# Kernel optimization log

Measured on AMD Instinct MI355X. Metric: run time of the kernel, lower is better.

## Reference

```python
import jax, jax.numpy as jnp
import numpy as np

RES = 14
KEY_DIM = 32
NUM_HEADS = 12
ATTN_RATIO = 4
DIM = 384
VAL_ATTN_DIM = ATTN_RATIO * KEY_DIM * NUM_HEADS  # 1536
QKV_DIM = VAL_ATTN_DIM + 2 * KEY_DIM * NUM_HEADS  # 2304
BN_EPS = 1e-5


def _bias_idxs():
    # torch.meshgrid default is 'ij'
    gy, gx = jnp.meshgrid(jnp.arange(RES), jnp.arange(RES), indexing='ij')
    pos = jnp.stack([gy.reshape(-1), gx.reshape(-1)])           # [2, N]
    rel = jnp.abs(pos[:, :, None] - pos[:, None, :])            # [2, N, N]
    return rel[0] * RES + rel[1]                                # [N, N] int


def _linear_bn(x, w, gamma, beta, mean, var):
    # bias-free Linear (torch weight layout [out,in]) + BatchNorm1d (eval)
    y = x @ w.T
    inv = gamma / jnp.sqrt(var + BN_EPS)
    return y * inv + (beta - mean * inv)


def setup_inputs() -> dict:
    key = jax.random.key(0)
    ks = jax.random.split(key, 12)
    B, N = 128, RES * RES
    f = jax.random.normal
    return {
        'x': f(ks[0], (B, N, DIM), jnp.float32),
        'qkv_w': f(ks[1], (QKV_DIM, DIM), jnp.float32) * 0.02,
        'qkv_gamma': f(ks[2], (QKV_DIM,), jnp.float32) * 0.1 + 1.0,
        'qkv_beta': f(ks[3], (QKV_DIM,), jnp.float32) * 0.1,
        'qkv_mean': f(ks[4], (QKV_DIM,), jnp.float32) * 0.1,
        'qkv_var': jax.random.uniform(ks[5], (QKV_DIM,), jnp.float32, 0.5, 1.5),
        'attn_biases': f(ks[6], (NUM_HEADS, RES * RES), jnp.float32) * 0.1,
        'proj_w': f(ks[7], (DIM, VAL_ATTN_DIM), jnp.float32) * 0.02,
        'proj_gamma': f(ks[8], (DIM,), jnp.float32) * 0.1 + 1.0,
        'proj_beta': f(ks[9], (DIM,), jnp.float32) * 0.1,
        'proj_mean': f(ks[10], (DIM,), jnp.float32) * 0.1,
        'proj_var': jax.random.uniform(ks[11], (DIM,), jnp.float32, 0.5, 1.5),
    }


def reference(x, qkv_w, qkv_gamma, qkv_beta, qkv_mean, qkv_var,
              attn_biases, proj_w, proj_gamma, proj_beta, proj_mean, proj_var):
    B, N, _ = x.shape
    scale = KEY_DIM ** -0.5
    qkv = _linear_bn(x, qkv_w, qkv_gamma, qkv_beta, qkv_mean, qkv_var)
    qkv = qkv.reshape(B, N, NUM_HEADS, -1)
    q = qkv[..., :KEY_DIM]                       # [B,N,H,dk]
    k = qkv[..., KEY_DIM:2 * KEY_DIM]            # [B,N,H,dk]
    v = qkv[..., 2 * KEY_DIM:]                   # [B,N,H,dv]
    bias = attn_biases[:, _bias_idxs()]          # [H,N,N]
    attn = jnp.einsum('bnhd,bmhd->bhnm', q, k) * scale + bias[None]
    attn = jax.nn.softmax(attn, axis=-1)
    out = jnp.einsum('bhnm,bmhd->bnhd', attn, v).reshape(B, N, VAL_ATTN_DIM)
    out = jax.nn.silu(out)
    return _linear_bn(out, proj_w, proj_gamma, proj_beta, proj_mean, proj_var)
```

## Files before the change

kernel.cpp:

```cpp
#include <hip/hip_runtime.h>
#include <cstdint>

#define NQ 196
#define DIMX 384
#define QKVD 2304
#define VAD 1536
#define NHD 12
#define MTOT 25088

#define KSTR 40
#define VSTR 232

typedef unsigned int u32;
typedef unsigned short u16;
typedef __bf16 bf16_t;
typedef bf16_t bf16x8 __attribute__((ext_vector_type(8)));
typedef float f32x4 __attribute__((ext_vector_type(4)));

__device__ inline u16 f2b(float f) {
  u32 u = __float_as_uint(f);
  u32 r = (u + 0x7fffu + ((u >> 16) & 1u)) >> 16;
  return (u16)r;
}
__device__ inline float b2f(u16 u) { return __uint_as_float(((u32)u) << 16); }
__device__ inline int iabs(int v) { return v < 0 ? -v : v; }

__device__ inline void gld_lds16(const void* g, void* l) {
  __builtin_amdgcn_global_load_lds((__attribute__((address_space(1))) void*)g,
                                   (__attribute__((address_space(3))) void*)l,
                                   16, 0, 0);
}


__global__ void cvt_kernel(const float* __restrict__ in, u16* __restrict__ out, int n4) {
  int i = blockIdx.x * 256 + threadIdx.x;
  if (i >= n4) return;
  float4 v = ((const float4*)in)[i];
  ushort4 o;
  o.x = f2b(v.x); o.y = f2b(v.y); o.z = f2b(v.z); o.w = f2b(v.w);
  ((ushort4*)out)[i] = o;
}

__global__ void bn_tab(const float* __restrict__ g, const float* __restrict__ be,
                       const float* __restrict__ mn, const float* __restrict__ vr,
                       float* __restrict__ inv, float* __restrict__ off, int n) {
  int i = blockIdx.x * 256 + threadIdx.x;
  if (i >= n) return;
  float iv = g[i] * rsqrtf(vr[i] + 1e-5f);
  inv[i] = iv;
  off[i] = be[i] - mn[i] * iv;
}


template <int MODE>
__global__ __launch_bounds__(256) void gemm_bt(
    const u16* __restrict__ A, const u16* __restrict__ B, int K,
    const float* __restrict__ inv, const float* __restrict__ off,
    u16* __restrict__ Qb, u16* __restrict__ Kb, u16* __restrict__ Vt,
    float* __restrict__ out) {
  __shared__ __align__(16) u16 As[128 * 32];
  __shared__ __align__(16) u16 Bs[128 * 32];
  const int tid = threadIdx.x;
  const int wid = tid >> 6, lane = tid & 63;
  const int wm = wid & 1, wn = wid >> 1;
  const int fr = lane & 15, fk = (lane >> 4) << 3;
  const u16* Ab = A + (size_t)(blockIdx.y * 128) * K;
  const u16* Bb = B + (size_t)(blockIdx.x * 128) * K;
  const int c0 = (wid << 6) | lane;
  const int r0 = c0 >> 2, kc0 = (c0 & 3) << 3;
  const int c1 = c0 + 256;
  const int r1 = c1 >> 2, kc1 = (c1 & 3) << 3;

  f32x4 acc[4][4] = {};

  for (int k0 = 0; k0 < K; k0 += 32) {
    gld_lds16(Ab + (size_t)r0 * K + (k0 + kc0), &As[wid << 9]);
    gld_lds16(Ab + (size_t)r1 * K + (k0 + kc1), &As[2048 + (wid << 9)]);
    gld_lds16(Bb + (size_t)r0 * K + (k0 + kc0), &Bs[wid << 9]);
    gld_lds16(Bb + (size_t)r1 * K + (k0 + kc1), &Bs[2048 + (wid << 9)]);
    __syncthreads();
    bf16x8 av[4], bv[4];
#pragma unroll
    for (int t = 0; t < 4; t++)
      av[t] = *(const bf16x8*)&As[(wm * 64 + t * 16 + fr) * 32 + fk];
#pragma unroll
    for (int t = 0; t < 4; t++)
      bv[t] = *(const bf16x8*)&Bs[(wn * 64 + t * 16 + fr) * 32 + fk];
#pragma unroll
    for (int mt = 0; mt < 4; mt++)
#pragma unroll
      for (int nt = 0; nt < 4; nt++)
        acc[mt][nt] = __builtin_amdgcn_mfma_f32_16x16x32_bf16(av[mt], bv[nt], acc[mt][nt], 0, 0, 0);
    __syncthreads();
  }

  const int colb = blockIdx.x * 128 + wn * 64 + fr;
  const int rowb = blockIdx.y * 128 + wm * 64 + ((lane >> 4) << 2);
#pragma unroll
  for (int nt = 0; nt < 4; nt++) {
    const int col = colb + nt * 16;
    const float iv = inv[col], of = off[col];
    if (MODE == 0) {
      const int h = col / 192, r = col - h * 192;
#pragma unroll
      for (int mt = 0; mt < 4; mt++)
#pragma unroll
        for (int rg = 0; rg < 4; rg++) {
          const int row = rowb + mt * 16 + rg;
          const float v = acc[mt][nt][rg] * iv + of;
          const int b = row / 196, n = row - b * 196;
          const size_t bh = (size_t)(b * NHD + h);
          const u16 us = f2b(v);
          if (r < 32) Qb[(bh * NQ + n) * 32 + r] = us;
          else if (r < 64) Kb[(bh * NQ + n) * 32 + (r - 32)] = us;
          else Vt[(bh * 128 + (r - 64)) * NQ + n] = us;
        }
    } else {
#pragma unroll
      for (int mt = 0; mt < 4; mt++)
#pragma unroll
        for (int rg = 0; rg < 4; rg++) {
          const int row = rowb + mt * 16 + rg;
          out[(size_t)row * DIMX + col] = acc[mt][nt][rg] * iv + of;
        }
    }
  }
}


__global__ __launch_bounds__(512) void attn_kernel(
    const u16* __restrict__ Qg, const u16* __restrict__ Kg,
    const u16* __restrict__ Vtg, const float* __restrict__ biases,
    u16* __restrict__ AO) {
  __shared__ __align__(16) u16 Ks[208 * KSTR];
  __shared__ __align__(16) u16 Vs[128 * VSTR];
  __shared__ __align__(16) u16 Ps[8][16 * VSTR];
  __shared__ __align__(16) float biasS[NQ];

  const int tid = threadIdx.x, wid = tid >> 6, lane = tid & 63;
  const int fr = lane & 15, fj = lane >> 4, fk = fj << 3;
  const int bh = blockIdx.x, b = bh / NHD, h = bh - b * NHD;
  const float scale = 0.17677669529663687f;

  for (int i = tid; i < NQ * 4; i += 512) {
    const int m = i >> 2, kc = (i & 3) << 3;
    uint4 v = *(const uint4*)(Kg + ((size_t)bh * NQ + m) * 32 + kc);
    *(uint4*)&Ks[m * KSTR + kc] = v;
  }
  {
    const u32* src = (const u32*)(Vtg + (size_t)bh * 128 * NQ);
    u32* dst = (u32*)Vs;
    for (int i = tid; i < 128 * 98; i += 512) {
      const int d = i / 98, nc = i - d * 98;
      dst[d * (VSTR / 2) + nc] = src[i];
    }
    for (int i = tid; i < 128 * 18; i += 512) {
      const int d = i / 18, nc = 98 + (i - d * 18);
      dst[d * (VSTR / 2) + nc] = 0u;
    }
  }
  if (tid < NQ) biasS[tid] = biases[h * NQ + tid];
  {
    const int row = lane >> 2, c = 208 + (lane & 3) * 4;
    *(uint2*)&Ps[wid][row * VSTR + c] = make_uint2(0u, 0u);
  }
  __syncthreads();

  for (int rt = wid; rt < 13; rt += 8) {
    int qrow = rt * 16 + fr; qrow = qrow > 195 ? 195 : qrow;
    const bf16x8 qf = *(const bf16x8*)(Qg + ((size_t)bh * NQ + qrow) * 32 + fk);

    f32x4 s[13];
#pragma unroll
    for (int t = 0; t < 13; t++) {
      const bf16x8 kf = *(const bf16x8*)&Ks[(t * 16 + fr) * KSTR + fk];
      f32x4 z = {0.f, 0.f, 0.f, 0.f};
      s[t] = __builtin_amdgcn_mfma_f32_16x16x32_bf16(qf, kf, z, 0, 0, 0);
    }

    int yn[4], xn[4];
#pragma unroll
    for (int rg = 0; rg < 4; rg++) {
      int n = rt * 16 + fj * 4 + rg;
      int y = (n * 586) >> 13; y = y > 13 ? 13 : y;
      yn[rg] = y; xn[rg] = n - y * 14;
    }
#pragma unroll
    for (int t = 0; t < 13; t++) {
      const int m = t * 16 + fr;
      const bool valid = m < NQ;
      int ym = (m * 586) >> 13; ym = ym > 13 ? 13 : ym;
      const int xm = m - ym * 14;
#pragma unroll
      for (int rg = 0; rg < 4; rg++) {
        int idx = iabs(yn[rg] - ym) * 14 + iabs(xn[rg] - xm);
        idx = idx > 195 ? 195 : idx;
        const float bv = biasS[idx];
        s[t][rg] = valid ? (s[t][rg] * scale + bv) : -1e30f;
      }
    }
    float rinv[4];
#pragma unroll
    for (int rg = 0; rg < 4; rg++) {
      float mx = s[0][rg];
#pragma unroll
      for (int t = 1; t < 13; t++) mx = fmaxf(mx, s[t][rg]);
      mx = fmaxf(mx, __shfl_xor(mx, 1));
      mx = fmaxf(mx, __shfl_xor(mx, 2));
      mx = fmaxf(mx, __shfl_xor(mx, 4));
      mx = fmaxf(mx, __shfl_xor(mx, 8));
      float ls = 0.f;
#pragma unroll
      for (int t = 0; t < 13; t++) {
        const float e = __expf(s[t][rg] - mx);
        s[t][rg] = e;
        ls += e;
      }
      ls += __shfl_xor(ls, 1);
      ls += __shfl_xor(ls, 2);
      ls += __shfl_xor(ls, 4);
      ls += __shfl_xor(ls, 8);
      rinv[rg] = 1.f / ls;
    }
#pragma unroll
    for (int t = 0; t < 13; t++)
#pragma unroll
      for (int rg = 0; rg < 4; rg++)
        Ps[wid][(fj * 4 + rg) * VSTR + t * 16 + fr] = f2b(s[t][rg]);
    __threadfence_block();

    f32x4 o[8] = {};
#pragma unroll
    for (int kc = 0; kc < 7; kc++) {
      const bf16x8 pf = *(const bf16x8*)&Ps[wid][fr * VSTR + kc * 32 + fk];
#pragma unroll
      for (int dt = 0; dt < 8; dt++) {
        const bf16x8 vf = *(const bf16x8*)&Vs[(dt * 16 + fr) * VSTR + kc * 32 + fk];
        o[dt] = __builtin_amdgcn_mfma_f32_16x16x32_bf16(pf, vf, o[dt], 0, 0, 0);
      }
    }
#pragma unroll
    for (int rg = 0; rg < 4; rg++) {
      const int n = rt * 16 + fj * 4 + rg;
      if (n < NQ) {
        const float rv = rinv[rg];
#pragma unroll
        for (int dt = 0; dt < 8; dt++) {
          float x = o[dt][rg] * rv;
          x = x / (1.f + __expf(-x));
          AO[((size_t)(b * NQ + n)) * VAD + h * 128 + dt * 16 + fr] = f2b(x);
        }
      }
    }
    __threadfence_block();
  }
}


extern "C" void kernel_launch(void* const* d_in, const int* in_sizes, int n_in,
                              void* d_out, int out_size, void* d_ws, size_t ws_size,
                              hipStream_t stream) {
  const float* x          = (const float*)d_in[0];
  const float* qkv_w      = (const float*)d_in[1];
  const float* qkv_gamma  = (const float*)d_in[2];
  const float* qkv_beta   = (const float*)d_in[3];
  const float* qkv_mean   = (const float*)d_in[4];
  const float* qkv_var    = (const float*)d_in[5];
  const float* attn_bias  = (const float*)d_in[6];
  const float* proj_w     = (const float*)d_in[7];
  const float* proj_gamma = (const float*)d_in[8];
  const float* proj_beta  = (const float*)d_in[9];
  const float* proj_mean  = (const float*)d_in[10];
  const float* proj_var   = (const float*)d_in[11];

  const size_t szXB    = (size_t)MTOT * DIMX * 2;
  const size_t szQKVW  = (size_t)QKVD * DIMX * 2;
  const size_t szPROJW = (size_t)DIMX * VAD * 2;
  const size_t szQK    = (size_t)128 * NHD * NQ * 32 * 2;
  const size_t szV     = (size_t)128 * NHD * 128 * NQ * 2;
  const size_t szAO    = (size_t)MTOT * VAD * 2;
  const size_t szX     = (szXB + szQKVW > szAO) ? (szXB + szQKVW) : szAO;

  char* w = (char*)d_ws;
  u16* projwb = (u16*)w; w += szPROJW;
  float* inv1 = (float*)w; w += QKVD * 4;
  float* off1 = (float*)w; w += QKVD * 4;
  float* inv2 = (float*)w; w += DIMX * 4;
  float* off2 = (float*)w; w += DIMX * 4;
  u16* Qb = (u16*)w; w += szQK;
  u16* Kb = (u16*)w; w += szQK;
  u16* Vt = (u16*)w; w += szV;
  char* regionX = w; w += szX;
  u16* xb    = (u16*)regionX;
  u16* qkvwb = (u16*)(regionX + szXB);
  u16* AO    = (u16*)regionX;

  if ((size_t)(w - (char*)d_ws) > ws_size) return;

  cvt_kernel<<<MTOT * DIMX / 4 / 256, 256, 0, stream>>>(x, xb, MTOT * DIMX / 4);
  cvt_kernel<<<QKVD * DIMX / 4 / 256, 256, 0, stream>>>(qkv_w, qkvwb, QKVD * DIMX / 4);
  cvt_kernel<<<DIMX * VAD / 4 / 256, 256, 0, stream>>>(proj_w, projwb, DIMX * VAD / 4);
  bn_tab<<<(QKVD + 255) / 256, 256, 0, stream>>>(qkv_gamma, qkv_beta, qkv_mean, qkv_var, inv1, off1, QKVD);
  bn_tab<<<(DIMX + 255) / 256, 256, 0, stream>>>(proj_gamma, proj_beta, proj_mean, proj_var, inv2, off2, DIMX);

  gemm_bt<0><<<dim3(QKVD / 128, MTOT / 128), 256, 0, stream>>>(
      xb, qkvwb, DIMX, inv1, off1, Qb, Kb, Vt, nullptr);
  attn_kernel<<<128 * NHD, 512, 0, stream>>>(Qb, Kb, Vt, attn_bias, AO);
  gemm_bt<1><<<dim3(DIMX / 128, MTOT / 128), 256, 0, stream>>>(
      AO, projwb, VAD, inv2, off2, nullptr, nullptr, nullptr, (float*)d_out);
}
```

Measured before the change: 442.0 us.

## Permute QKV weight columns and stage GEMM epilogue through LDS for coalesced stores

The QKV weight rows and BN tables are reordered so each 128-column GEMM tile holds only Q heads, only K heads, or a single V head. The epilogue then writes the tile into LDS, transposed for V, and copies it out with vectorized, coalesced 16-byte or 8-byte stores. This replaces the scattered 2-byte stores, including the strided V-transpose writes, that the old epilogue issued. In exchange the QKV GEMM uses more LDS (a 128x140 staging tile) and needs an extra barrier, which may lower occupancy.

Result: faster. 401.6 us (-9.2%).

```diff
diff --git a/kernel.cpp b/kernel.cpp
--- a/kernel.cpp
+++ b/kernel.cpp
@@ -10,6 +10,7 @@
 
 #define KSTR 40
 #define VSTR 232
+#define TSTR 140
 
 typedef unsigned int u32;
 typedef unsigned short u16;
@@ -39,6 +40,21 @@
   ushort4 o;
   o.x = f2b(v.x); o.y = f2b(v.y); o.z = f2b(v.z); o.w = f2b(v.w);
   ((ushort4*)out)[i] = o;
+}
+
+__global__ void cvt_wqkv(const float* __restrict__ in, u16* __restrict__ out) {
+  int i = blockIdx.x * 256 + threadIdx.x;
+  if (i >= QKVD * DIMX / 4) return;
+  const int newc = i / (DIMX / 4);
+  const int kc = (i - newc * (DIMX / 4)) * 4;
+  int oldc;
+  if (newc < 384)      { int h = newc >> 5;              oldc = h * 192 + (newc & 31); }
+  else if (newc < 768) { int t = newc - 384; int h = t >> 5; oldc = h * 192 + 32 + (t & 31); }
+  else                 { int t = newc - 768; int h = t >> 7; oldc = h * 192 + 64 + (t & 127); }
+  float4 v = *(const float4*)(in + (size_t)oldc * DIMX + kc);
+  ushort4 o;
+  o.x = f2b(v.x); o.y = f2b(v.y); o.z = f2b(v.z); o.w = f2b(v.w);
+  *(ushort4*)(out + (size_t)newc * DIMX + kc) = o;
 }
 
 __global__ void bn_tab(const float* __restrict__ g, const float* __restrict__ be,
@@ -51,6 +67,20 @@
   off[i] = be[i] - mn[i] * iv;
 }
 
+__global__ void bn_tab_qkv(const float* __restrict__ g, const float* __restrict__ be,
+                           const float* __restrict__ mn, const float* __restrict__ vr,
+                           float* __restrict__ inv, float* __restrict__ off) {
+  int i = blockIdx.x * 256 + threadIdx.x;
+  if (i >= QKVD) return;
+  const int h = i / 192, r = i - h * 192;
+  const int newc = (r < 32) ? h * 32 + r
+                 : (r < 64) ? 384 + h * 32 + (r - 32)
+                            : 768 + h * 128 + (r - 64);
+  float iv = g[i] * rsqrtf(vr[i] + 1e-5f);
+  inv[newc] = iv;
+  off[newc] = be[i] - mn[i] * iv;
+}
+
 
 template <int MODE>
 __global__ __launch_bounds__(256) void gemm_bt(
@@ -58,8 +88,10 @@
     const float* __restrict__ inv, const float* __restrict__ off,
     u16* __restrict__ Qb, u16* __restrict__ Kb, u16* __restrict__ Vt,
     float* __restrict__ out) {
-  __shared__ __align__(16) u16 As[128 * 32];
-  __shared__ __align__(16) u16 Bs[128 * 32];
+  constexpr int LDSU = (MODE == 0) ? 128 * TSTR : 8192;
+  __shared__ __align__(16) u16 lds[LDSU];
+  u16* As = lds;
+  u16* Bs = lds + 4096;
   const int tid = threadIdx.x;
   const int wid = tid >> 6, lane = tid & 63;
   const int wm = wid & 1, wn = wid >> 1;
@@ -94,28 +126,62 @@
     __syncthreads();
   }
 
-  const int colb = blockIdx.x * 128 + wn * 64 + fr;
-  const int rowb = blockIdx.y * 128 + wm * 64 + ((lane >> 4) << 2);
-#pragma unroll
-  for (int nt = 0; nt < 4; nt++) {
-    const int col = colb + nt * 16;
-    const float iv = inv[col], of = off[col];
-    if (MODE == 0) {
-      const int h = col / 192, r = col - h * 192;
+  const int lrow0 = wm * 64 + ((lane >> 4) << 2);
+  const int lcol0 = wn * 64 + fr;
+
+  if (MODE == 0) {
+    const int bx = blockIdx.x, by = blockIdx.y;
+    const bool isV = bx >= 6;
+#pragma unroll
+    for (int nt = 0; nt < 4; nt++) {
+      const int lc = lcol0 + nt * 16;
+      const int gc = bx * 128 + lc;
+      const float iv = inv[gc], of = off[gc];
 #pragma unroll
       for (int mt = 0; mt < 4; mt++)
 #pragma unroll
         for (int rg = 0; rg < 4; rg++) {
-          const int row = rowb + mt * 16 + rg;
-          const float v = acc[mt][nt][rg] * iv + of;
-          const int b = row / 196, n = row - b * 196;
-          const size_t bh = (size_t)(b * NHD + h);
-          const u16 us = f2b(v);
-          if (r < 32) Qb[(bh * NQ + n) * 32 + r] = us;
-          else if (r < 64) Kb[(bh * NQ + n) * 32 + (r - 32)] = us;
-          else Vt[(bh * 128 + (r - 64)) * NQ + n] = us;
+          const int lr = lrow0 + mt * 16 + rg;
+          const u16 us = f2b(acc[mt][nt][rg] * iv + of);
+          if (isV) lds[lc * TSTR + lr] = us;
+          else     lds[lr * TSTR + lc] = us;
         }
+    }
+    __syncthreads();
+    if (!isV) {
+      u16* dstB = (bx < 3) ? Qb : Kb;
+      const int h0 = (bx < 3 ? bx : bx - 3) * 4;
+#pragma unroll
+      for (int it = 0; it < 8; it++) {
+        const int idx = it * 256 + tid;
+        const int ch = idx & 3, hl = (idx >> 2) & 3, row = idx >> 4;
+        const int rowg = by * 128 + row;
+        const int b = rowg / 196, n = rowg - b * 196;
+        const size_t bh = (size_t)(b * NHD + h0 + hl);
+        const u16* src = &lds[row * TSTR + hl * 32 + ch * 8];
+        uint2 a0 = *(const uint2*)src;
+        uint2 a1 = *(const uint2*)(src + 4);
+        *(uint4*)(dstB + (bh * NQ + n) * 32 + ch * 8) = make_uint4(a0.x, a0.y, a1.x, a1.y);
+      }
     } else {
+      const int h = bx - 6;
+#pragma unroll
+      for (int it = 0; it < 16; it++) {
+        const int idx = it * 256 + tid;
+        const int nk = idx & 31, col = idx >> 5;
+        const int rowg = by * 128 + nk * 4;
+        const int b = rowg / 196, n = rowg - b * 196;
+        uint2 v = *(const uint2*)&lds[col * TSTR + nk * 4];
+        *(uint2*)(Vt + ((size_t)(b * NHD + h) * 128 + col) * NQ + n) = v;
+      }
+    }
+  } else {
+    const int colb = blockIdx.x * 128 + lcol0;
+    const int rowb = blockIdx.y * 128 + lrow0;
+#pragma unroll
+    for (int nt = 0; nt < 4; nt++) {
+      const int col = colb + nt * 16;
+      const float iv = inv[col], of = off[col];
 #pragma unroll
       for (int mt = 0; mt < 4; mt++)
 #pragma unroll
@@ -298,9 +364,9 @@
   if ((size_t)(w - (char*)d_ws) > ws_size) return;
 
   cvt_kernel<<<MTOT * DIMX / 4 / 256, 256, 0, stream>>>(x, xb, MTOT * DIMX / 4);
-  cvt_kernel<<<QKVD * DIMX / 4 / 256, 256, 0, stream>>>(qkv_w, qkvwb, QKVD * DIMX / 4);
+  cvt_wqkv<<<(QKVD * DIMX / 4 + 255) / 256, 256, 0, stream>>>(qkv_w, qkvwb);
   cvt_kernel<<<DIMX * VAD / 4 / 256, 256, 0, stream>>>(proj_w, projwb, DIMX * VAD / 4);
-  bn_tab<<<(QKVD + 255) / 256, 256, 0, stream>>>(qkv_gamma, qkv_beta, qkv_mean, qkv_var, inv1, off1, QKVD);
+  bn_tab_qkv<<<(QKVD + 255) / 256, 256, 0, stream>>>(qkv_gamma, qkv_beta, qkv_mean, qkv_var, inv1, off1);
   bn_tab<<<(DIMX + 255) / 256, 256, 0, stream>>>(proj_gamma, proj_beta, proj_mean, proj_var, inv2, off2, DIMX);
 
   gemm_bt<0><<<dim3(QKVD / 128, MTOT / 128), 256, 0, stream>>>(
```
